# Kernel optimization log

Measured on AMD Instinct MI355X. Metric: run time of the kernel, lower is better.

## Reference

```python
import jax, jax.numpy as jnp
import numpy as np

B, S, DIM = 1, 2048, 2048
NH, NKV, HD = 32, 8, 64
NREP = NH // NKV  # 4


def setup_inputs() -> dict:
    key = jax.random.key(0)
    ks = jax.random.split(key, 5)
    x = jax.random.normal(ks[0], (B, S, DIM), jnp.float32)
    # torch nn.Linear weight layout: (out_features, in_features)
    wq = jax.random.normal(ks[1], (NH * HD, DIM), jnp.float32) * (DIM ** -0.5)
    wk = jax.random.normal(ks[2], (NKV * HD, DIM), jnp.float32) * (DIM ** -0.5)
    wv = jax.random.normal(ks[3], (NKV * HD, DIM), jnp.float32) * (DIM ** -0.5)
    wo = jax.random.normal(ks[4], (DIM, NH * HD), jnp.float32) * ((NH * HD) ** -0.5)
    # Llama-style rotary frequencies: angle[t, i] = t / 10000^(2i/head_dim)
    inv_freq = 1.0 / (10000.0 ** (np.arange(0, HD, 2, dtype=np.float64) / HD))  # (HD/2,)
    ang = np.outer(np.arange(S, dtype=np.float64), inv_freq)                     # (S, HD/2)
    freqs_cis = jnp.asarray(np.stack([np.cos(ang), np.sin(ang)], axis=-1), jnp.float32)  # (S, HD/2, 2)
    # additive causal mask, shape (1, 1, S, S)
    mask = jnp.triu(jnp.full((S, S), -1e9, jnp.float32), k=1)[None, None]
    return dict(x=x, wq=wq, wk=wk, wv=wv, wo=wo, freqs_cis=freqs_cis, mask=mask)


def _apply_rope(x, cos, sin):
    # x: (B, S, H, HD); rotate adjacent pairs along last dim
    xr = x.reshape(x.shape[:-1] + (-1, 2))
    x1, x2 = xr[..., 0], xr[..., 1]
    c = cos[None, :, None, :]  # (1, S, 1, HD/2)
    s = sin[None, :, None, :]
    out = jnp.stack([x1 * c - x2 * s, x1 * s + x2 * c], axis=-1)
    return out.reshape(x.shape)


def reference(x, wq, wk, wv, wo, freqs_cis, mask):
    b, s, _ = x.shape
    q = (x @ wq.T).reshape(b, s, NH, HD)
    k = (x @ wk.T).reshape(b, s, NKV, HD)
    v = (x @ wv.T).reshape(b, s, NKV, HD)
    cos, sin = freqs_cis[..., 0], freqs_cis[..., 1]
    q = _apply_rope(q, cos, sin)
    k = _apply_rope(k, cos, sin)
    # GQA: group q heads by kv head instead of materializing repeated K/V
    qg = q.reshape(b, s, NKV, NREP, HD)
    scale = HD ** -0.5
    # scores: (b, g=kv_head, r=rep, s=q_pos, t=k_pos)
    scores = jnp.einsum('bsgrd,btgd->bgrst', qg, k) * scale
    scores = scores + mask[:, :, None]  # (1,1,1,S,S) broadcast
    p = jax.nn.softmax(scores.astype(jnp.float32), axis=-1).astype(q.dtype)
    out = jnp.einsum('bgrst,btgd->bsgrd', p, v).reshape(b, s, NH * HD)
    return out @ wo.T
```

## Files before the change

### kernel.cpp

```cpp
#include <hip/hip_runtime.h>
#include <hip/hip_bf16.h>

#define S_LEN 2048
#define DIM_  2048
#define NH    32
#define NKV   8
#define HD    64

typedef __bf16 bf16x8 __attribute__((ext_vector_type(8)));
typedef __bf16 bf16x4 __attribute__((ext_vector_type(4)));
typedef float  f32x4  __attribute__((ext_vector_type(4)));

#define AS_GLOBAL(p) ((const __attribute__((address_space(1))) void*)(p))
#define AS_LDS(p)    ((__attribute__((address_space(3))) void*)(p))

__device__ __forceinline__ bf16x8 pack8(float4 a, float4 b) {
  bf16x8 r;
  r[0] = (__bf16)a.x; r[1] = (__bf16)a.y; r[2] = (__bf16)a.z; r[3] = (__bf16)a.w;
  r[4] = (__bf16)b.x; r[5] = (__bf16)b.y; r[6] = (__bf16)b.z; r[7] = (__bf16)b.w;
  return r;
}

__global__ __launch_bounds__(256) void cvt_xw(
    const float* __restrict__ x,  const float* __restrict__ wq,
    const float* __restrict__ wk, const float* __restrict__ wv,
    const float* __restrict__ wo,
    __bf16* __restrict__ xb, __bf16* __restrict__ wb, __bf16* __restrict__ wob)
{
  const size_t stride = 458752;
  size_t base = (size_t)blockIdx.x * 256 + threadIdx.x;
#pragma unroll
  for (int k = 0; k < 4; ++k) {
    size_t i = base + (size_t)k * stride;
    const float* src; __bf16* dst; size_t j;
    if (i < 524288)       { src = x;  dst = xb;            j = i; }
    else if (i < 1048576) { src = wq; dst = wb;            j = i - 524288; }
    else if (i < 1179648) { src = wk; dst = wb + 4194304;  j = i - 1048576; }
    else if (i < 1310720) { src = wv; dst = wb + 5242880;  j = i - 1179648; }
    else                  { src = wo; dst = wob;           j = i - 1310720; }
    float4 f0 = ((const float4*)src)[j * 2];
    float4 f1 = ((const float4*)src)[j * 2 + 1];
    ((bf16x8*)dst)[j ^ ((j >> 8) & 7)] = pack8(f0, f1);
  }
}

#define BK 64
#define TA_ELEMS 8192
#define TB_ELEMS 4096

__device__ __forceinline__ void stage_A(
    const __bf16* __restrict__ g, int row0, int k0, int ld, __bf16* lds)
{
  const int tid = threadIdx.x;
  const int wave = tid >> 6;
#pragma unroll
  for (int iss = 0; iss < 4; ++iss) {
    int off = (iss * 256 + tid) * 16;
    int r = off >> 7;
    int c = (off & 127) >> 1;
    __builtin_amdgcn_global_load_lds(
        AS_GLOBAL(g + (size_t)(row0 + r) * ld + k0 + c),
        AS_LDS(lds + iss * 2048 + wave * 512), 16, 0, 0);
  }
}

__device__ __forceinline__ void stage_B(
    const __bf16* __restrict__ g, int row0, int k0, int ld, __bf16* lds)
{
  const int tid = threadIdx.x;
  const int wave = tid >> 6;
#pragma unroll
  for (int iss = 0; iss < 2; ++iss) {
    int off = (iss * 256 + tid) * 16;
    int r = off >> 7;
    int c = (off & 127) >> 1;
    __builtin_amdgcn_global_load_lds(
        AS_GLOBAL(g + (size_t)(row0 + r) * ld + k0 + c),
        AS_LDS(lds + iss * 2048 + wave * 512), 16, 0, 0);
  }
}

__device__ __forceinline__ void gemm_mainloop(
    const __bf16* __restrict__ A, const __bf16* __restrict__ B,
    int row0, int col0, int lda, int ldb, int nt,
    __bf16* As, __bf16* Bs, f32x4 acc[4][2])
{
  const int lane = threadIdx.x & 63;
  const int wave = threadIdx.x >> 6;
  const int wr = wave >> 1, wc = wave & 1;
  const int fr = lane & 15, fg = lane >> 4;
  const int sw = fr & 7;

  stage_A(A, row0, 0, lda, As);
  stage_B(B, col0, 0, ldb, Bs);

  for (int t = 0; t < nt; ++t) {
    const int cur = t & 1;

    asm volatile("" ::: "memory");
    __builtin_amdgcn_s_barrier();
    asm volatile("" ::: "memory");

    const int tn = (t + 1 < nt) ? t + 1 : t;
    stage_A(A, row0, tn * BK, lda, As + (cur ^ 1) * TA_ELEMS);
    stage_B(B, col0, tn * BK, ldb, Bs + (cur ^ 1) * TB_ELEMS);

    asm volatile("s_waitcnt vmcnt(6)" ::: "memory");

    __builtin_amdgcn_s_barrier();
    asm volatile("" ::: "memory");

#pragma unroll
    for (int kk = 0; kk < 2; ++kk) {
      bf16x8 a[4], b[2];
#pragma unroll
      for (int mi = 0; mi < 4; ++mi)
        a[mi] = *(const bf16x8*)(As + cur * TA_ELEMS +
                 (wr * 64 + mi * 16 + fr) * 64 + (((kk * 4 + fg) ^ sw) * 8));
#pragma unroll
      for (int ni = 0; ni < 2; ++ni)
        b[ni] = *(const bf16x8*)(Bs + cur * TB_ELEMS +
                 (wc * 32 + ni * 16 + fr) * 64 + (((kk * 4 + fg) ^ sw) * 8));
#pragma unroll
      for (int mi = 0; mi < 4; ++mi)
#pragma unroll
        for (int ni = 0; ni < 2; ++ni)
          acc[mi][ni] = __builtin_amdgcn_mfma_f32_16x16x32_bf16(a[mi], b[ni], acc[mi][ni], 0, 0, 0);
    }
  }
}

__global__ __launch_bounds__(256) void qkv_gemm(
    const __bf16* __restrict__ xb, const __bf16* __restrict__ wb,
    const float* __restrict__ fc,
    __bf16* __restrict__ q_buf, __bf16* __restrict__ k_buf, __bf16* __restrict__ v_buf)
{
  __shared__ __bf16 As[2 * TA_ELEMS];
  __shared__ __bf16 Bs[2 * TB_ELEMS];
  const int lane = threadIdx.x & 63;
  const int wave = threadIdx.x >> 6;
  const int wr = wave >> 1, wc = wave & 1;
  const int fr = lane & 15, fg = lane >> 4;

  const int lid = blockIdx.x;
  const int xcd = lid & 7;
  const int i   = lid >> 3;
  const int row0 = (i & 15) * 128;
  const int col0 = (xcd * 6 + (i >> 4)) * 64;

  f32x4 acc[4][2] = {};
  gemm_mainloop(xb, wb, row0, col0, DIM_, DIM_, DIM_ / BK, As, Bs, acc);

  const int rowg0 = row0 + wr * 64;
  const int colg0 = col0 + wc * 32;
#pragma unroll
  for (int mi = 0; mi < 4; ++mi) {
#pragma unroll
    for (int ni = 0; ni < 2; ++ni) {
#pragma unroll
      for (int j = 0; j < 4; ++j) {
        int row = rowg0 + mi * 16 + fg * 4 + j;
        int col = colg0 + ni * 16 + fr;
        float v = acc[mi][ni][j];
        if (col < 2048) {
          int h = col >> 6, d = col & 63;
          q_buf[((size_t)h * S_LEN + row) * HD + d] = (__bf16)v;
        } else if (col < 2560) {
          int c = col - 2048, g = c >> 6, d = c & 63;
          float vp = __shfl_xor(v, 1, 64);
          const float* cs = fc + ((size_t)row * 32 + (d >> 1)) * 2;
          float cc = cs[0], ss = cs[1];
          float vr = (d & 1) ? (vp * ss + v * cc) : (v * cc - vp * ss);
          k_buf[((size_t)g * S_LEN + row) * HD + d] = (__bf16)vr;
        } else {
          int c = col - 2560, g = c >> 6, d = c & 63;
          v_buf[((size_t)g * HD + d) * S_LEN + row] = (__bf16)v;
        }
      }
    }
  }
}

__global__ __launch_bounds__(256) void oproj_gemm(
    const __bf16* __restrict__ attn_buf, const __bf16* __restrict__ wob,
    float* __restrict__ out)
{
  __shared__ __bf16 As[2 * TA_ELEMS];
  __shared__ __bf16 Bs[2 * TB_ELEMS];
  const int lane = threadIdx.x & 63;
  const int wave = threadIdx.x >> 6;
  const int wr = wave >> 1, wc = wave & 1;
  const int fr = lane & 15, fg = lane >> 4;

  const int lid = blockIdx.x;
  const int xcd = lid & 7;
  const int i   = lid >> 3;
  const int row0 = (i & 15) * 128;
  const int col0 = (xcd * 4 + (i >> 4)) * 64;

  f32x4 acc[4][2] = {};
  gemm_mainloop(attn_buf, wob, row0, col0, DIM_, DIM_, DIM_ / BK, As, Bs, acc);

  const int rowg0 = row0 + wr * 64;
  const int colg0 = col0 + wc * 32;
#pragma unroll
  for (int mi = 0; mi < 4; ++mi)
#pragma unroll
    for (int ni = 0; ni < 2; ++ni)
#pragma unroll
      for (int j = 0; j < 4; ++j) {
        int row = rowg0 + mi * 16 + fg * 4 + j;
        int col = colg0 + ni * 16 + fr;
        out[(size_t)row * DIM_ + col] = acc[mi][ni][j];
      }
}

__global__ __launch_bounds__(512) void attn_kernel(
    const __bf16* __restrict__ q_buf, const __bf16* __restrict__ k_buf,
    const __bf16* __restrict__ v_buf, const float* __restrict__ fc,
    __bf16* __restrict__ attn_buf)
{
  __shared__ __align__(16) __bf16 Ks[2][64 * 64];
  __shared__ __align__(16) __bf16 Vs[2][64 * 64];
  __shared__ __align__(16) __bf16 lds_p[8][16][72];

  const int tid  = threadIdx.x;
  const int lane = tid & 63;
  const int wave = tid >> 6;
  const int n = blockIdx.x;
  const int qt = (n < 256) ? (15 - (n >> 5)) : ((n - 256) >> 5);
  const int h  = n & 31;
  const int g = h >> 2;
  const int r0 = qt * 128 + wave * 16;
  const int lrow = lane & 15;
  const int lgrp = lane >> 4;
  const int lk = lgrp * 8;

  const __bf16* qh = q_buf + (size_t)h * S_LEN * HD;
  const __bf16* kh = k_buf + (size_t)g * S_LEN * HD;
  const __bf16* vh = v_buf + (size_t)g * HD * S_LEN;

  const int sr   = tid >> 3;
  const int scol = tid & 7;
  const int dcol = scol ^ (sr & 7);

  const float KS = 0.125f * 1.44269504088896f;
  bf16x8 qa[2];
  const float* fcrow = fc + (size_t)(r0 + lrow) * 64;
#pragma unroll
  for (int kk = 0; kk < 2; ++kk) {
    qa[kk] = *(const bf16x8*)(qh + (size_t)(r0 + lrow) * HD + kk * 32 + lk);
    float4 cs0 = *(const float4*)(fcrow + (kk * 16 + lgrp * 4) * 2);
    float4 cs1 = *(const float4*)(fcrow + (kk * 16 + lgrp * 4) * 2 + 4);
    float cc[4] = {cs0.x * KS, cs0.z * KS, cs1.x * KS, cs1.z * KS};
    float ss[4] = {cs0.y * KS, cs0.w * KS, cs1.y * KS, cs1.w * KS};
#pragma unroll
    for (int pr = 0; pr < 4; ++pr) {
      float x1 = (float)qa[kk][2 * pr], x2 = (float)qa[kk][2 * pr + 1];
      qa[kk][2 * pr]     = (__bf16)(x1 * cc[pr] - x2 * ss[pr]);
      qa[kk][2 * pr + 1] = (__bf16)(x1 * ss[pr] + x2 * cc[pr]);
    }
  }

  bf16x8 vones;
#pragma unroll
  for (int i = 0; i < 8; ++i) vones[i] = (__bf16)1.0f;

  f32x4 oacc[5] = {};

  const int nt = 2 * qt + 2;

  {
    uint4 k0 = *(const uint4*)(kh + (size_t)sr * HD + scol * 8);
    uint4 v0 = *(const uint4*)(vh + (size_t)sr * S_LEN + scol * 8);
    *(uint4*)(&Ks[0][sr * 64 + dcol * 8]) = k0;
    *(uint4*)(&Vs[0][sr * 64 + dcol * 8]) = v0;
  }
  __syncthreads();

  for (int t = 0; t < nt; ++t) {
    const int cur = t & 1;
    const int t0 = t * 64;

    const int tn0 = (t + 1 < nt ? t + 1 : t) * 64;
    uint4 kreg = *(const uint4*)(kh + (size_t)(tn0 + sr) * HD + scol * 8);
    uint4 vreg = *(const uint4*)(vh + (size_t)sr * S_LEN + tn0 + scol * 8);

    const int dmax = r0 + 15 - t0;
    if (dmax >= 0) {
      f32x4 sc[4] = {};
      const int cmax = dmax >> 4;
      __builtin_amdgcn_s_setprio(1);
#pragma unroll
      for (int c = 0; c < 4; ++c) {
        if (c <= cmax) {
#pragma unroll
          for (int kk = 0; kk < 2; ++kk) {
            bf16x8 ka = *(const bf16x8*)(
                &Ks[cur][(c * 16 + lrow) * 64 + (((kk * 4 + lgrp) ^ (lrow & 7)) * 8)]);
            sc[c] = __builtin_amdgcn_mfma_f32_16x16x32_bf16(ka, qa[kk], sc[c], 0, 0, 0);
          }
        }
      }
      __builtin_amdgcn_s_setprio(0);

      float p[16];
      const int q = r0 + lrow;
      if (t0 + 63 <= r0) {
#pragma unroll
        for (int c = 0; c < 4; ++c)
#pragma unroll
          for (int j = 0; j < 4; ++j)
            p[c * 4 + j] = __builtin_amdgcn_exp2f(sc[c][j]);
      } else {
#pragma unroll
        for (int c = 0; c < 4; ++c)
#pragma unroll
          for (int j = 0; j < 4; ++j) {
            int kv = t0 + c * 16 + lgrp * 4 + j;
            p[c * 4 + j] = (kv <= q) ? __builtin_amdgcn_exp2f(sc[c][j]) : 0.0f;
          }
      }

#pragma unroll
      for (int c = 0; c < 4; ++c)
#pragma unroll
        for (int e = 0; e < 2; ++e) {
          union { __bf16 hh[2]; unsigned u; } pk;
          pk.hh[0] = (__bf16)p[c * 4 + 2 * e];
          pk.hh[1] = (__bf16)p[c * 4 + 2 * e + 1];
          *(unsigned*)&lds_p[wave][lrow][c * 16 + lgrp * 4 + 2 * e] = pk.u;
        }
      asm volatile("s_waitcnt lgkmcnt(0)" ::: "memory");

      bf16x8 pa0 = *(const bf16x8*)&lds_p[wave][lrow][lk];
      __builtin_amdgcn_s_setprio(1);
#pragma unroll
      for (int nf = 0; nf < 4; ++nf) {
        bf16x8 vb = *(const bf16x8*)(
            &Vs[cur][(nf * 16 + lrow) * 64 + ((lgrp ^ (lrow & 7)) * 8)]);
        oacc[nf] = __builtin_amdgcn_mfma_f32_16x16x32_bf16(pa0, vb, oacc[nf], 0, 0, 0);
      }
      oacc[4] = __builtin_amdgcn_mfma_f32_16x16x32_bf16(pa0, vones, oacc[4], 0, 0, 0);
      __builtin_amdgcn_s_setprio(0);
      if (dmax >= 32) {
        bf16x8 pa1 = *(const bf16x8*)&lds_p[wave][lrow][32 + lk];
        __builtin_amdgcn_s_setprio(1);
#pragma unroll
        for (int nf = 0; nf < 4; ++nf) {
          bf16x8 vb = *(const bf16x8*)(
              &Vs[cur][(nf * 16 + lrow) * 64 + (((4 + lgrp) ^ (lrow & 7)) * 8)]);
          oacc[nf] = __builtin_amdgcn_mfma_f32_16x16x32_bf16(pa1, vb, oacc[nf], 0, 0, 0);
        }
        oacc[4] = __builtin_amdgcn_mfma_f32_16x16x32_bf16(pa1, vones, oacc[4], 0, 0, 0);
        __builtin_amdgcn_s_setprio(0);
      }
    }

    *(uint4*)(&Ks[cur ^ 1][sr * 64 + dcol * 8]) = kreg;
    *(uint4*)(&Vs[cur ^ 1][sr * 64 + dcol * 8]) = vreg;
    __syncthreads();
  }

  float rlr[4];
#pragma unroll
  for (int j = 0; j < 4; ++j)
    rlr[j] = 1.0f / oacc[4][j];
#pragma unroll
  for (int nf = 0; nf < 4; ++nf)
#pragma unroll
    for (int j = 0; j < 4; ++j) {
      int row = r0 + lgrp * 4 + j;
      int col = h * HD + nf * 16 + lrow;
      int ch  = (((col >> 3) & 7) ^ (row & 7));
      int cols = (col & 7) | (ch << 3) | (col & ~63);
      attn_buf[(size_t)row * (NH * HD) + cols] =
          (__bf16)(oacc[nf][j] * rlr[j]);
    }
}

extern "C" void kernel_launch(void* const* d_in, const int* in_sizes, int n_in,
                              void* d_out, int out_size, void* d_ws, size_t ws_size,
                              hipStream_t stream)
{
  const float* x  = (const float*)d_in[0];
  const float* wq = (const float*)d_in[1];
  const float* wk = (const float*)d_in[2];
  const float* wv = (const float*)d_in[3];
  const float* wo = (const float*)d_in[4];
  const float* fc = (const float*)d_in[5];
  float* out = (float*)d_out;

  char* ws = (char*)d_ws;
  __bf16* q_buf    = (__bf16*)(ws);
  __bf16* k_buf    = (__bf16*)(ws +  8u * 1024 * 1024);
  __bf16* v_buf    = (__bf16*)(ws + 10u * 1024 * 1024);
  __bf16* attn_buf = (__bf16*)(ws + 12u * 1024 * 1024);
  __bf16* xb       = (__bf16*)(ws + 20u * 1024 * 1024);
  __bf16* wb       = (__bf16*)(ws + 28u * 1024 * 1024);
  __bf16* wob      = (__bf16*)(ws + 40u * 1024 * 1024);

  cvt_xw<<<dim3(1792), 256, 0, stream>>>(x, wq, wk, wv, wo, xb, wb, wob);
  qkv_gemm<<<dim3(768), 256, 0, stream>>>(xb, wb, fc, q_buf, k_buf, v_buf);
  attn_kernel<<<dim3(512), 512, 0, stream>>>(q_buf, k_buf, v_buf, fc, attn_buf);
  oproj_gemm<<<dim3(512), 256, 0, stream>>>(attn_buf, wob, out);
}
```

Measured before the change: 121.7 us.

## Pre-swizzle K/V in global memory and stream attention tiles via direct-to-LDS loads

Measured after the change: 131.0 us. +7.6%, slower.

```diff
diff --git a/kernel.cpp b/kernel.cpp
--- a/kernel.cpp
+++ b/kernel.cpp
@@ -106,10 +106,10 @@
     stage_B(B, col0, tn * BK, ldb, Bs + (cur ^ 1) * TB_ELEMS);
 
     asm volatile("s_waitcnt vmcnt(6)" ::: "memory");
-
     __builtin_amdgcn_s_barrier();
     asm volatile("" ::: "memory");
 
+    __builtin_amdgcn_s_setprio(1);
 #pragma unroll
     for (int kk = 0; kk < 2; ++kk) {
       bf16x8 a[4], b[2];
@@ -127,6 +127,7 @@
         for (int ni = 0; ni < 2; ++ni)
           acc[mi][ni] = __builtin_amdgcn_mfma_f32_16x16x32_bf16(a[mi], b[ni], acc[mi][ni], 0, 0, 0);
     }
+    __builtin_amdgcn_s_setprio(0);
   }
 }
 
@@ -171,10 +172,12 @@
           const float* cs = fc + ((size_t)row * 32 + (d >> 1)) * 2;
           float cc = cs[0], ss = cs[1];
           float vr = (d & 1) ? (vp * ss + v * cc) : (v * cc - vp * ss);
-          k_buf[((size_t)g * S_LEN + row) * HD + d] = (__bf16)vr;
+          int ds = (d & 7) | ((((d >> 3) & 7) ^ (row & 7)) << 3);
+          k_buf[((size_t)g * S_LEN + row) * HD + ds] = (__bf16)vr;
         } else {
           int c = col - 2560, g = c >> 6, d = c & 63;
-          v_buf[((size_t)g * HD + d) * S_LEN + row] = (__bf16)v;
+          int kvs = (row & 7) | ((((row >> 3) & 7) ^ (d & 7)) << 3) | (row & ~63);
+          v_buf[((size_t)g * HD + d) * S_LEN + kvs] = (__bf16)v;
         }
       }
     }
@@ -240,9 +243,8 @@
   const __bf16* kh = k_buf + (size_t)g * S_LEN * HD;
   const __bf16* vh = v_buf + (size_t)g * HD * S_LEN;
 
-  const int sr   = tid >> 3;
-  const int scol = tid & 7;
-  const int dcol = scol ^ (sr & 7);
+  const int vrow = tid >> 3;
+  const int vsl  = (tid & 7) * 8;
 
   const float KS = 0.125f * 1.44269504088896f;
   bf16x8 qa[2];
@@ -270,21 +272,32 @@
 
   const int nt = 2 * qt + 2;
 
-  {
-    uint4 k0 = *(const uint4*)(kh + (size_t)sr * HD + scol * 8);
-    uint4 v0 = *(const uint4*)(vh + (size_t)sr * S_LEN + scol * 8);
-    *(uint4*)(&Ks[0][sr * 64 + dcol * 8]) = k0;
-    *(uint4*)(&Vs[0][sr * 64 + dcol * 8]) = v0;
-  }
-  __syncthreads();
+  __builtin_amdgcn_global_load_lds(
+      AS_GLOBAL(kh + tid * 8),
+      AS_LDS(&Ks[0][wave * 512]), 16, 0, 0);
+  __builtin_amdgcn_global_load_lds(
+      AS_GLOBAL(vh + (size_t)vrow * S_LEN + vsl),
+      AS_LDS(&Vs[0][wave * 512]), 16, 0, 0);
 
   for (int t = 0; t < nt; ++t) {
     const int cur = t & 1;
     const int t0 = t * 64;
 
+    asm volatile("" ::: "memory");
+    __builtin_amdgcn_s_barrier();
+    asm volatile("" ::: "memory");
+
     const int tn0 = (t + 1 < nt ? t + 1 : t) * 64;
-    uint4 kreg = *(const uint4*)(kh + (size_t)(tn0 + sr) * HD + scol * 8);
-    uint4 vreg = *(const uint4*)(vh + (size_t)sr * S_LEN + tn0 + scol * 8);
+    __builtin_amdgcn_global_load_lds(
+        AS_GLOBAL(kh + (size_t)tn0 * HD + tid * 8),
+        AS_LDS(&Ks[cur ^ 1][wave * 512]), 16, 0, 0);
+    __builtin_amdgcn_global_load_lds(
+        AS_GLOBAL(vh + (size_t)vrow * S_LEN + tn0 + vsl),
+        AS_LDS(&Vs[cur ^ 1][wave * 512]), 16, 0, 0);
+
+    asm volatile("s_waitcnt vmcnt(2)" ::: "memory");
+    __builtin_amdgcn_s_barrier();
+    asm volatile("" ::: "memory");
 
     const int dmax = r0 + 15 - t0;
     if (dmax >= 0) {
@@ -323,14 +336,14 @@
       }
 
 #pragma unroll
-      for (int c = 0; c < 4; ++c)
-#pragma unroll
-        for (int e = 0; e < 2; ++e) {
-          union { __bf16 hh[2]; unsigned u; } pk;
-          pk.hh[0] = (__bf16)p[c * 4 + 2 * e];
-          pk.hh[1] = (__bf16)p[c * 4 + 2 * e + 1];
-          *(unsigned*)&lds_p[wave][lrow][c * 16 + lgrp * 4 + 2 * e] = pk.u;
-        }
+      for (int c = 0; c < 4; ++c) {
+        union { __bf16 hh[4]; unsigned long long u; } pk;
+        pk.hh[0] = (__bf16)p[c * 4 + 0];
+        pk.hh[1] = (__bf16)p[c * 4 + 1];
+        pk.hh[2] = (__bf16)p[c * 4 + 2];
+        pk.hh[3] = (__bf16)p[c * 4 + 3];
+        *(unsigned long long*)&lds_p[wave][lrow][c * 16 + lgrp * 4] = pk.u;
+      }
       asm volatile("s_waitcnt lgkmcnt(0)" ::: "memory");
 
       bf16x8 pa0 = *(const bf16x8*)&lds_p[wave][lrow][lk];
@@ -356,10 +369,6 @@
         __builtin_amdgcn_s_setprio(0);
       }
     }
-
-    *(uint4*)(&Ks[cur ^ 1][sr * 64 + dcol * 8]) = kreg;
-    *(uint4*)(&Vs[cur ^ 1][sr * 64 + dcol * 8]) = vreg;
-    __syncthreads();
   }
 
   float rlr[4];
```
